# Performance work log

Hardware: AMD Instinct MI355X
Metric: run time of the kernel (lower is better)

## Reference

```python
import jax, jax.numpy as jnp
import numpy as np

GRID_SIZE = 5
SPLINE_ORDER = 3
NUM_BASIS = GRID_SIZE + SPLINE_ORDER  # 8
BN_EPS = 1e-5


def make_grid():
    # efficient_kan extended uniform grid on [-1, 1]
    h = 2.0 / GRID_SIZE
    return (jnp.arange(-SPLINE_ORDER, GRID_SIZE + SPLINE_ORDER + 1, dtype=jnp.float32) * h) - 1.0


def b_splines(x, grid):
    """Cox-de Boor B-spline bases. x: (...,) -> (..., NUM_BASIS)."""
    x = x[..., None]
    bases = ((x >= grid[:-1]) & (x < grid[1:])).astype(x.dtype)
    for p in range(1, SPLINE_ORDER + 1):
        left = (x - grid[: -(p + 1)]) / (grid[p:-1] - grid[: -(p + 1)])
        right = (grid[p + 1:] - x) / (grid[p + 1:] - grid[1:-p])
        bases = left * bases[..., :-1] + right * bases[..., 1:]
    return bases


def grouped_conv(x, w, groups, padding):
    return jax.lax.conv_general_dilated(
        x, w, window_strides=(1, 1), padding=[(padding, padding)] * 2,
        feature_group_count=groups,
        dimension_numbers=("NCHW", "OIHW", "NCHW"))


def kan_conv(x, w_base, b_base, w_spline, grid, groups, padding):
    # base branch: grouped conv on SiLU(x)
    base = grouped_conv(jax.nn.silu(x), w_base, groups, padding)
    base = base + b_base[None, :, None, None]
    # spline branch: per-channel B-spline basis expansion (C -> C*NUM_BASIS)
    B, C, H, W = x.shape
    sp = b_splines(jnp.moveaxis(x, 1, -1), grid)            # (B,H,W,C,NB)
    sp = jnp.moveaxis(sp.reshape(B, H, W, C * NUM_BASIS), -1, 1)  # (B,C*NB,H,W)
    return base + grouped_conv(sp, w_spline, groups, padding)


def setup_inputs() -> dict:
    key = jax.random.key(0)
    ks = jax.random.split(key, 8)
    B, C_in, C_out, G, H, W = 16, 128, 256, 8, 64, 64
    x = jax.random.normal(ks[0], (B, C_in, H, W), dtype=jnp.float32)
    w_base1 = jax.random.normal(ks[1], (C_out, C_in // G, 1, 1), jnp.float32) * 0.1
    b_base1 = jnp.zeros((C_out,), jnp.float32)
    w_spline1 = jax.random.normal(ks[2], (C_out, (C_in * NUM_BASIS) // G, 1, 1), jnp.float32) * 0.05
    w_base2 = jax.random.normal(ks[3], (C_out, C_out // G, 3, 3), jnp.float32) * 0.05
    b_base2 = jnp.zeros((C_out,), jnp.float32)
    w_spline2 = jax.random.normal(ks[4], (C_out, (C_out * NUM_BASIS) // G, 3, 3), jnp.float32) * 0.02
    gamma = jnp.ones((C_out,), jnp.float32)
    beta = jnp.zeros((C_out,), jnp.float32)
    return {"x": x, "w_base1": w_base1, "b_base1": b_base1, "w_spline1": w_spline1,
            "w_base2": w_base2, "b_base2": b_base2, "w_spline2": w_spline2,
            "gamma": gamma, "beta": beta}


def reference(x, w_base1, b_base1, w_spline1, w_base2, b_base2, w_spline2, gamma, beta):
    G = 8
    grid = make_grid()
    h = kan_conv(x, w_base1, b_base1, w_spline1, grid, G, padding=0)   # 1x1 grouped KAN conv
    h = kan_conv(h, w_base2, b_base2, w_spline2, grid, G, padding=1)   # 3x3 grouped KAN conv
    # BatchNorm2d (training mode: batch statistics over N,H,W)
    mean = jnp.mean(h, axis=(0, 2, 3), keepdims=True)
    var = jnp.var(h, axis=(0, 2, 3), keepdims=True)
    hn = (h - mean) * jax.lax.rsqrt(var + BN_EPS)
    return hn * gamma[None, :, None, None] + beta[None, :, None, None]
```

## Files before the change

### kernel.cpp

```cpp
#include <hip/hip_runtime.h>
#include <hip/hip_bf16.h>
#include <stdint.h>


#define NB 8
#define NF 9
#define CIN 128
#define COUT 256
#define GROUPS 8
#define HW 4096
#define BATCH 16

#define WFS_ELEMS 589824
#define WFB_ELEMS 73728
#define WF1S_ELEMS 32768
#define WF1B_ELEMS 8192

typedef __attribute__((ext_vector_type(8))) short bf16x8;
typedef __attribute__((ext_vector_type(4))) float f32x4;

__device__ __forceinline__ unsigned bf16r(float f) {
    union { float f; unsigned u; } c; c.f = f;
    unsigned r = c.u + 0x7FFF + ((c.u >> 16) & 1);
    return r >> 16;
}
__device__ __forceinline__ unsigned bfpack2(float lo, float hi) {
    unsigned r;
    asm("v_cvt_pk_bf16_f32 %0, %1, %2" : "=v"(r) : "v"(lo), "v"(hi));
    return r;
}
__device__ __forceinline__ unsigned bfpack2_typed(float lo, float hi) {
    __hip_bfloat16 a = __float2bfloat16(lo);
    __hip_bfloat16 b = __float2bfloat16(hi);
    unsigned short ua, ub;
    __builtin_memcpy(&ua, &a, 2);
    __builtin_memcpy(&ub, &b, 2);
    return (unsigned)ua | ((unsigned)ub << 16);
}

__device__ __forceinline__ float silu_fast(float v) {
    float e = __builtin_amdgcn_exp2f(v * -1.44269504088896f);
    return v * __builtin_amdgcn_rcpf(1.0f + e);
}

__device__ __forceinline__ void spline_w(float v, float& w0, float& w1,
                                         float& w2, float& w3, int& k) {
    float s = (v + 2.2f) * 2.5f;
    float fk = floorf(s);
    k = (int)fk;
    float u = s - fk;
    float um = 1.0f - u;
    float u2 = u * u, u3 = u2 * u;
    w0 = um * um * um * (1.0f / 6.0f);
    w1 = (3.0f * u3 - 6.0f * u2 + 4.0f) * (1.0f / 6.0f);
    w2 = (-3.0f * u3 + 3.0f * u2 + 3.0f * u + 1.0f) * (1.0f / 6.0f);
    w3 = u3 * (1.0f / 6.0f);
}

__device__ __forceinline__ uint4 spline_row(float v, bool in, float& sv) {
    sv = silu_fast(v);
    float w0, w1, w2, w3; int k;
    spline_w(v, w0, w1, w2, w3, k);
    unsigned W0 = bfpack2(w0, w1);
    unsigned W1 = bfpack2(w2, w3);
    int kk = in ? (k - 3) : 99;
    unsigned odd = (unsigned)kk & 1u;
    unsigned A = W0 << 16;
    unsigned B = (W0 >> 16) | (W1 << 16);
    unsigned C = W1 >> 16;
    unsigned t0 = odd ? A : W0;
    unsigned t1 = odd ? B : W1;
    unsigned t2 = odd ? C : 0u;
    int q = kk >> 1;
    uint4 pk;
    pk.x = (q == 0) ? t0 : (q == -1) ? t1 : (q == -2) ? t2 : 0u;
    pk.y = (q == 1) ? t0 : (q == 0)  ? t1 : (q == -1) ? t2 : 0u;
    pk.z = (q == 2) ? t0 : (q == 1)  ? t1 : (q == 0)  ? t2 : 0u;
    pk.w = (q == 3) ? t0 : (q == 2)  ? t1 : (q == 1)  ? t2 : 0u;
    return pk;
}

__device__ __forceinline__ void expand_u(int raw, bool in,
                                         uint4& pk, unsigned& su) {
    float v = __uint_as_float(((unsigned)raw) << 16);
    float sv;
    pk = spline_row(v, in, sv);
    su = bf16r(sv);
}

__global__ void __launch_bounds__(256) repack2_kernel(
    const float* __restrict__ wb1, const float* __restrict__ ws1,
    const float* __restrict__ wb2, const float* __restrict__ ws2,
    unsigned short* __restrict__ wfs, unsigned short* __restrict__ wfb,
    unsigned short* __restrict__ wf1s, unsigned short* __restrict__ wf1b) {
    int i = blockIdx.x * 256 + threadIdx.x;
    if (i < WF1S_ELEMS) {
        int j = i & 7;
        int lane = (i >> 3) & 63;
        int nf = (i >> 9) & 1;
        int cc = (i >> 10) & 3;
        int g = i >> 12;
        int c_loc = cc * 4 + (lane >> 4);
        int cog = g * 32 + nf * 16 + (lane & 15);
        wf1s[i] = (unsigned short)bf16r(ws1[cog * 128 + c_loc * 8 + j]);
    }
    if (i < WF1B_ELEMS) {
        int j = i & 7;
        int lane = (i >> 3) & 63;
        int nf = (i >> 9) & 1;
        int g = (i >> 10) & 7;
        int k = (lane >> 4) * 8 + j;
        int cog = g * 32 + nf * 16 + (lane & 15);
        wf1b[i] = (k < 16) ? (unsigned short)bf16r(wb1[cog * 16 + k]) : 0;
    }
    if (i < WFB_ELEMS) {
        int j = i & 7;
        int lane = (i >> 3) & 63;
        int nf = (i >> 9) & 1;
        int t = i >> 10;
        int dy = t % 3; t /= 3;
        int dx = t % 3; t /= 3;
        int g = t;
        int ch = (lane >> 4) * 8 + j;
        int cog = g * 32 + nf * 16 + (lane & 15);
        wfb[i] = (unsigned short)bf16r(wb2[((cog * 32 + ch) * 3 + dy) * 3 + dx]);
    }
    if (i < WFS_ELEMS) {
        int j = i & 7;
        int t = i >> 3;
        int lane = t & 63; t >>= 6;
        int nf = t & 1; t >>= 1;
        int dy = t % 3; t /= 3;
        int dx = t % 3; t /= 3;
        int cc = t & 7; t >>= 3;
        int g = t;
        int c_loc = cc * 4 + (lane >> 4);
        int cog = g * 32 + nf * 16 + (lane & 15);
        float v = ws2[((cog * 256 + c_loc * 8 + j) * 3 + dy) * 3 + dx];
        wfs[i] = (unsigned short)bf16r(v);
    }
}

__global__ void __launch_bounds__(256, 4) kan1m_kernel(
    const float* __restrict__ x, const bf16x8* __restrict__ wf1s,
    const bf16x8* __restrict__ wf1b, const float* __restrict__ bb1,
    unsigned short* __restrict__ h1) {
    __shared__ __align__(16) unsigned char lds[32768];
    unsigned char* spl = lds;
    unsigned char* slu = lds + 16384;

    const int tid = threadIdx.x;
    const int lane = tid & 63;
    const int w = tid >> 6;
    const int blk = blockIdx.x;
    const int tile = blk & 15;
    const int g = (blk >> 4) & 7;
    const int b = blk >> 7;
    const int lrow = lane & 15;
    const int lhi = lane >> 4;
    const int posg0 = tile * 256;

    {
        int key = (tid >> 1) & 3;
        uint4 z = {0, 0, 0, 0};
        *reinterpret_cast<uint4*>(slu + tid * 64 + ((2 ^ key) << 4)) = z;
        *reinterpret_cast<uint4*>(slu + tid * 64 + ((3 ^ key) << 4)) = z;
    }

    const float* xg = x + ((size_t)b * CIN + g * 16) * HW + posg0;

    float xreg[4];
#pragma unroll
    for (int it = 0; it < 4; ++it) xreg[it] = xg[it * HW + tid];

    f32x4 acc[4][2];
#pragma unroll
    for (int m = 0; m < 4; ++m)
#pragma unroll
        for (int nf = 0; nf < 2; ++nf) {
            float bias = bb1[g * 32 + nf * 16 + lrow];
            acc[m][nf] = (f32x4){bias, bias, bias, bias};
        }

    for (int cc = 0; cc < 4; ++cc) {
        __syncthreads();
        int key = (tid >> 1) & 3;
#pragma unroll
        for (int it = 0; it < 4; ++it) {
            float sv;
            uint4 pk = spline_row(xreg[it], true, sv);
            *reinterpret_cast<uint4*>(spl + tid * 64 + ((it ^ key) << 4)) = pk;
            int cg = cc * 4 + it;
            *reinterpret_cast<unsigned short*>(
                slu + tid * 64 + (((cg >> 3) ^ key) << 4) + (cg & 7) * 2) =
                (unsigned short)bf16r(sv);
        }
        if (cc < 3) {
#pragma unroll
            for (int it = 0; it < 4; ++it)
                xreg[it] = xg[((cc + 1) * 4 + it) * HW + tid];
        }
        __syncthreads();
        const bf16x8* wpc = wf1s + (size_t)((g * 4 + cc) * 2) * 64;
        bf16x8 bf0 = wpc[lane];
        bf16x8 bf1 = wpc[64 + lane];
#pragma unroll
        for (int m = 0; m < 4; ++m) {
            int pos = w * 64 + m * 16 + lrow;
            int ra = pos * 64 + ((lhi ^ ((pos >> 1) & 3)) << 4);
            bf16x8 af = *reinterpret_cast<const bf16x8*>(spl + ra);
            acc[m][0] = __builtin_amdgcn_mfma_f32_16x16x32_bf16(af, bf0, acc[m][0], 0, 0, 0);
            acc[m][1] = __builtin_amdgcn_mfma_f32_16x16x32_bf16(af, bf1, acc[m][1], 0, 0, 0);
        }
    }
    {
        const bf16x8* wpb = wf1b + (size_t)(g * 2) * 64;
        bf16x8 bf0 = wpb[lane];
        bf16x8 bf1 = wpb[64 + lane];
#pragma unroll
        for (int m = 0; m < 4; ++m) {
            int pos = w * 64 + m * 16 + lrow;
            int ra = pos * 64 + ((lhi ^ ((pos >> 1) & 3)) << 4);
            bf16x8 af = *reinterpret_cast<const bf16x8*>(slu + ra);
            acc[m][0] = __builtin_amdgcn_mfma_f32_16x16x32_bf16(af, bf0, acc[m][0], 0, 0, 0);
            acc[m][1] = __builtin_amdgcn_mfma_f32_16x16x32_bf16(af, bf1, acc[m][1], 0, 0, 0);
        }
    }
#pragma unroll
    for (int m = 0; m < 4; ++m)
#pragma unroll
        for (int nf = 0; nf < 2; ++nf) {
            int co = g * 32 + nf * 16 + lrow;
            size_t base = ((size_t)b * COUT + co) * HW + posg0 + w * 64 + m * 16 + lhi * 4;
            uint2 o = {bfpack2_typed(acc[m][nf][0], acc[m][nf][1]),
                       bfpack2_typed(acc[m][nf][2], acc[m][nf][3])};
            *reinterpret_cast<uint2*>(&h1[base]) = o;
        }
}

__device__ __forceinline__ void mfma_hr(
    const unsigned char* __restrict__ base, const int (&ra)[6],
    const bf16x8 (&bf)[3][2], f32x4 (&acc)[4][2]) {
#pragma unroll
    for (int hr = 0; hr < 6; ++hr) {
        bf16x8 af = *reinterpret_cast<const bf16x8*>(base + ra[hr]);
#pragma unroll
        for (int dy = 0; dy < 3; ++dy) {
            int y = hr - dy;
            if (y >= 0 && y < 4) {
                acc[y][0] = __builtin_amdgcn_mfma_f32_16x16x32_bf16(af, bf[dy][0], acc[y][0], 0, 0, 0);
                acc[y][1] = __builtin_amdgcn_mfma_f32_16x16x32_bf16(af, bf[dy][1], acc[y][1], 0, 0, 0);
            }
        }
    }
}

__global__ void __launch_bounds__(256, 3) kan2_mfma5_kernel(
    const unsigned short* __restrict__ h1, const bf16x8* __restrict__ wfs,
    const bf16x8* __restrict__ wfb, const float* __restrict__ bb2,
    unsigned short* __restrict__ hb, float* __restrict__ partial2) {
    __shared__ __align__(16) unsigned char lds[41472];
    unsigned char* spl = lds;
    unsigned char* slu = lds + 20736;

    const int tid = threadIdx.x;
    const int lane = tid & 63;
    const int w = tid >> 6;
    const int blk = blockIdx.x;
    const int tile = blk & 15;
    const int g = (blk >> 4) & 7;
    const int b = blk >> 7;
    const int ty = (tile >> 2) * 16, tx = (tile & 3) * 16;
    const int lrow = lane & 15;
    const int lhi = lane >> 4;

    int offv[6], wadS[6], sluB[6], keysh[6];
#pragma unroll
    for (int it = 0; it < 6; ++it) {
        int e = tid + it * 256;
        int ch = (e * 3237) >> 20;
        int p = e - ch * 324;
        int hy = (p * 57) >> 10;
        int hx = p - hy * 18;
        int iy = ty + hy - 1, ix = tx + hx - 1;
        bool in = ((unsigned)iy < 64u) & ((unsigned)ix < 64u);
        offv[it] = in ? (ch * HW + iy * 64 + ix) : -1;
        int key = (p >> 1) & 3;
        wadS[it] = p * 64 + ((ch ^ key) << 4);
        sluB[it] = p * 64 + ch * 2;
        keysh[it] = key << 4;
    }

    const int pbase0 = (w * 4) * 18 + lrow;
    int raA[3][6];
#pragma unroll
    for (int dx = 0; dx < 3; ++dx)
#pragma unroll
        for (int hr = 0; hr < 6; ++hr) {
            int p = pbase0 + dx + hr * 18;
            raA[dx][hr] = p * 64 + ((lhi ^ ((p >> 1) & 3)) << 4);
        }

    const unsigned short* h1g = h1 + (size_t)(b * COUT + g * 32) * HW;

    int vregU[6];
    uint4 ereg[6];
    unsigned sreg[6];
#pragma unroll
    for (int it = 0; it < 6; ++it)
        if (it < 5 || tid < 16)
            vregU[it] = (offv[it] >= 0) ? (int)h1g[offv[it]] : 0;
#pragma unroll
    for (int it = 0; it < 6; ++it)
        if (it < 5 || tid < 16)
            expand_u(vregU[it], offv[it] >= 0, ereg[it], sreg[it]);
#pragma unroll
    for (int it = 0; it < 6; ++it)
        if (it < 5 || tid < 16)
            vregU[it] = (offv[it] >= 0) ? (int)h1g[4 * HW + offv[it]] : 0;

    f32x4 acc[4][2];
#pragma unroll
    for (int y = 0; y < 4; ++y)
#pragma unroll
        for (int nf = 0; nf < 2; ++nf) {
            float bias = bb2[g * 32 + nf * 16 + lrow];
            acc[y][nf] = (f32x4){bias, bias, bias, bias};
        }

    const bf16x8* wl = wfs + (size_t)(g * 8) * 18 * 64 + lane;

    for (int cc = 0; cc < 8; ++cc) {
        bf16x8 bf0[3][2];
#pragma unroll
        for (int dy = 0; dy < 3; ++dy)
#pragma unroll
            for (int nf = 0; nf < 2; ++nf)
                bf0[dy][nf] = wl[(dy * 2 + nf) * 64];

        __syncthreads();
        {
            int t4 = (cc >> 1) << 4;
            int u8 = (cc & 1) << 3;
#pragma unroll
            for (int it = 0; it < 6; ++it)
                if (it < 5 || tid < 16) {
                    *reinterpret_cast<uint4*>(spl + wadS[it]) = ereg[it];
                    *reinterpret_cast<unsigned short*>(
                        slu + sluB[it] + (t4 ^ keysh[it]) + u8) =
                        (unsigned short)sreg[it];
                }
        }
        __syncthreads();

        bf16x8 bf1[3][2], bf2[3][2];
#pragma unroll
        for (int dy = 0; dy < 3; ++dy)
#pragma unroll
            for (int nf = 0; nf < 2; ++nf)
                bf1[dy][nf] = wl[(6 + dy * 2 + nf) * 64];
        __builtin_amdgcn_s_setprio(1);
        mfma_hr(spl, raA[0], bf0, acc);
        __builtin_amdgcn_s_setprio(0);
#pragma unroll
        for (int dy = 0; dy < 3; ++dy)
#pragma unroll
            for (int nf = 0; nf < 2; ++nf)
                bf2[dy][nf] = wl[(12 + dy * 2 + nf) * 64];
        __builtin_amdgcn_s_setprio(1);
        mfma_hr(spl, raA[1], bf1, acc);
        __builtin_amdgcn_s_setprio(0);
        if (cc < 7) {
#pragma unroll
            for (int it = 0; it < 6; ++it)
                if (it < 5 || tid < 16)
                    expand_u(vregU[it], offv[it] >= 0, ereg[it], sreg[it]);
        }
        if (cc < 6) {
#pragma unroll
            for (int it = 0; it < 6; ++it)
                if (it < 5 || tid < 16)
                    vregU[it] = (offv[it] >= 0)
                        ? (int)h1g[(size_t)((cc + 2) * 4) * HW + offv[it]] : 0;
        }
        __builtin_amdgcn_s_setprio(1);
        mfma_hr(spl, raA[2], bf2, acc);
        __builtin_amdgcn_s_setprio(0);
        wl += 18 * 64;
    }

    {
        const bf16x8* wlb = wfb + (size_t)(g * 3) * 6 * 64 + lane;
#pragma unroll
        for (int dx = 0; dx < 3; ++dx) {
            bf16x8 bf[3][2];
#pragma unroll
            for (int dy = 0; dy < 3; ++dy)
#pragma unroll
                for (int nf = 0; nf < 2; ++nf)
                    bf[dy][nf] = wlb[(dx * 6 + dy * 2 + nf) * 64];
            __builtin_amdgcn_s_setprio(1);
            mfma_hr(slu, raA[dx], bf, acc);
            __builtin_amdgcn_s_setprio(0);
        }
    }

#pragma unroll
    for (int y = 0; y < 4; ++y) {
        int oy = ty + w * 4 + y;
#pragma unroll
        for (int nf = 0; nf < 2; ++nf) {
            int co = g * 32 + nf * 16 + lrow;
            uint2 o = {bfpack2_typed(acc[y][nf][0], acc[y][nf][1]),
                       bfpack2_typed(acc[y][nf][2], acc[y][nf][3])};
            *reinterpret_cast<uint2*>(
                &hb[(((size_t)b * COUT + co) * 64 + oy) * 64 + tx + lhi * 4]) = o;
        }
    }

    float s0 = 0.0f, q0 = 0.0f, s1 = 0.0f, q1 = 0.0f;
#pragma unroll
    for (int y = 0; y < 4; ++y)
#pragma unroll
        for (int i = 0; i < 4; ++i) {
            float a0 = acc[y][0][i], a1 = acc[y][1][i];
            s0 += a0; q0 = fmaf(a0, a0, q0);
            s1 += a1; q1 = fmaf(a1, a1, q1);
        }
    s0 += __shfl_xor(s0, 16); s0 += __shfl_xor(s0, 32);
    q0 += __shfl_xor(q0, 16); q0 += __shfl_xor(q0, 32);
    s1 += __shfl_xor(s1, 16); s1 += __shfl_xor(s1, 32);
    q1 += __shfl_xor(q1, 16); q1 += __shfl_xor(q1, 32);
    __syncthreads();
    float* stb = reinterpret_cast<float*>(lds);
    if (lane < 16) {
        int base = (w * 16 + lane) * 4;
        stb[base] = s0; stb[base + 1] = q0;
        stb[base + 2] = s1; stb[base + 3] = q1;
    }
    __syncthreads();
    if (tid < 64) {
        int slot = tid >> 1;
        int j = tid & 1;
        int lr = slot & 15, nf = slot >> 4;
        float a = 0.0f;
#pragma unroll
        for (int wv = 0; wv < 4; ++wv)
            a += stb[(wv * 16 + lr) * 4 + nf * 2 + j];
        partial2[blk * 64 + tid] = a;
    }
}

__global__ void __launch_bounds__(256) bnstat2_kernel(
    const float* __restrict__ partial2, const float* __restrict__ gamma,
    const float* __restrict__ beta, float* __restrict__ stats) {
    int co = blockIdx.x;
    int t = threadIdx.x;
    int g = co >> 5, loc = co & 31;
    int b = t >> 4, tile = t & 15;
    int blk = (b * 8 + g) * 16 + tile;
    float s = partial2[blk * 64 + loc * 2];
    float ss = partial2[blk * 64 + loc * 2 + 1];
    __shared__ float r1[256], r2[256];
    r1[t] = s; r2[t] = ss;
    __syncthreads();
    for (int o = 128; o > 0; o >>= 1) {
        if (t < o) { r1[t] += r1[t + o]; r2[t] += r2[t + o]; }
        __syncthreads();
    }
    if (t == 0) {
        const float invn = 1.0f / 65536.0f;
        float mean = r1[0] * invn;
        float var = r2[0] * invn - mean * mean;
        float sc = gamma[co] * rsqrtf(var + 1e-5f);
        stats[2 * co] = sc;
        stats[2 * co + 1] = beta[co] - mean * sc;
    }
}

__global__ void __launch_bounds__(256) bnapply_kernel(
    const unsigned short* __restrict__ hb, const float* __restrict__ stats,
    float* __restrict__ out) {
    int i = blockIdx.x * 256 + threadIdx.x;
    int co = (i >> 9) & 255;
    float sc = stats[2 * co], sh = stats[2 * co + 1];
    uint4 v = *reinterpret_cast<const uint4*>(hb + (size_t)i * 8);
    float4 o0, o1;
    o0.x = fmaf(__uint_as_float(v.x << 16), sc, sh);
    o0.y = fmaf(__uint_as_float(v.x & 0xFFFF0000u), sc, sh);
    o0.z = fmaf(__uint_as_float(v.y << 16), sc, sh);
    o0.w = fmaf(__uint_as_float(v.y & 0xFFFF0000u), sc, sh);
    o1.x = fmaf(__uint_as_float(v.z << 16), sc, sh);
    o1.y = fmaf(__uint_as_float(v.z & 0xFFFF0000u), sc, sh);
    o1.z = fmaf(__uint_as_float(v.w << 16), sc, sh);
    o1.w = fmaf(__uint_as_float(v.w & 0xFFFF0000u), sc, sh);
    float4* op = reinterpret_cast<float4*>(out + (size_t)i * 8);
    op[0] = o0;
    op[1] = o1;
}

extern "C" void kernel_launch(void* const* d_in, const int* in_sizes, int n_in,
                              void* d_out, int out_size, void* d_ws, size_t ws_size,
                              hipStream_t stream) {
    const float* x   = (const float*)d_in[0];
    const float* wb1 = (const float*)d_in[1];
    const float* bb1 = (const float*)d_in[2];
    const float* ws1 = (const float*)d_in[3];
    const float* wb2 = (const float*)d_in[4];
    const float* bb2 = (const float*)d_in[5];
    const float* ws2 = (const float*)d_in[6];
    const float* gamma = (const float*)d_in[7];
    const float* beta  = (const float*)d_in[8];

    char* ws = (char*)d_ws;
    unsigned short* wfs  = (unsigned short*)ws;
    unsigned short* wfb  = (unsigned short*)(ws + 1179648);
    unsigned short* wf1s = (unsigned short*)(ws + 1327104);
    unsigned short* wf1b = (unsigned short*)(ws + 1392640);
    float* partial2 = (float*)(ws + 1409024);
    float* stats    = (float*)(ws + 1933312);
    unsigned short* h1 = (unsigned short*)(ws + 1935360);
    unsigned short* hb = (unsigned short*)(ws + 35489792);

    repack2_kernel<<<(WFS_ELEMS + 255) / 256, 256, 0, stream>>>(
        wb1, ws1, wb2, ws2, wfs, wfb, wf1s, wf1b);
    kan1m_kernel<<<BATCH * GROUPS * 16, 256, 0, stream>>>(
        x, (const bf16x8*)wf1s, (const bf16x8*)wf1b, bb1, h1);
    kan2_mfma5_kernel<<<BATCH * GROUPS * 16, 256, 0, stream>>>(
        h1, (const bf16x8*)wfs, (const bf16x8*)wfb, bb2, hb, partial2);
    bnstat2_kernel<<<COUT, 256, 0, stream>>>(partial2, gamma, beta, stats);
    bnapply_kernel<<<8192, 256, 0, stream>>>(hb, stats, (float*)d_out);
}
```

Measured before the change: 148.6 us.

## Halve SiLU LDS buffer by splitting base-branch conv into two K16 MFMA passes

The SiLU staging buffer in LDS shrinks from 32 to 16 channels per pixel. The base-branch 3x3 conv is split into two halves: channels 0-15 run mid-loop at cc==3, before the buffer is overwritten, and channels 16-31 run after the loop. Both halves use 16x16x16 bf16 MFMAs, and the base weights are repacked to match. The smaller LDS footprint allows launch bounds of 4 blocks per CU instead of 3. The cost is more, smaller MFMA instructions and tighter register limits.

```diff
diff --git a/kernel.cpp b/kernel.cpp
--- a/kernel.cpp
+++ b/kernel.cpp
@@ -17,6 +17,7 @@
 #define WF1B_ELEMS 8192
 
 typedef __attribute__((ext_vector_type(8))) short bf16x8;
+typedef __attribute__((ext_vector_type(4))) short bf16x4;
 typedef __attribute__((ext_vector_type(4))) float f32x4;
 
 __device__ __forceinline__ unsigned bf16r(float f) {
@@ -36,6 +37,15 @@
     __builtin_memcpy(&ua, &a, 2);
     __builtin_memcpy(&ub, &b, 2);
     return (unsigned)ua | ((unsigned)ub << 16);
+}
+
+__device__ __forceinline__ f32x4 mfma16(bf16x4 a, bf16x4 b, f32x4 c) {
+#if __has_builtin(__builtin_amdgcn_mfma_f32_16x16x16bf16_1k)
+    return __builtin_amdgcn_mfma_f32_16x16x16bf16_1k(a, b, c, 0, 0, 0);
+#else
+    asm("v_mfma_f32_16x16x16_bf16 %0, %1, %2, %0" : "+v"(c) : "v"(a), "v"(b));
+    return c;
+#endif
 }
 
 __device__ __forceinline__ float silu_fast(float v) {
@@ -114,14 +124,15 @@
         wf1b[i] = (k < 16) ? (unsigned short)bf16r(wb1[cog * 16 + k]) : 0;
     }
     if (i < WFB_ELEMS) {
-        int j = i & 7;
-        int lane = (i >> 3) & 63;
-        int nf = (i >> 9) & 1;
-        int t = i >> 10;
+        int j = i & 3;
+        int lane = (i >> 2) & 63;
+        int nf = (i >> 8) & 1;
+        int t = i >> 9;
         int dy = t % 3; t /= 3;
         int dx = t % 3; t /= 3;
+        int half = t & 1; t >>= 1;
         int g = t;
-        int ch = (lane >> 4) * 8 + j;
+        int ch = half * 16 + (lane >> 4) * 4 + j;
         int cog = g * 32 + nf * 16 + (lane & 15);
         wfb[i] = (unsigned short)bf16r(wb2[((cog * 32 + ch) * 3 + dy) * 3 + dx]);
     }
@@ -255,11 +266,11 @@
     }
 }
 
-__global__ void __launch_bounds__(256, 3) kan2_mfma5_kernel(
+__global__ void __launch_bounds__(256, 4) kan2_mfma6_kernel(
     const unsigned short* __restrict__ h1, const bf16x8* __restrict__ wfs,
-    const bf16x8* __restrict__ wfb, const float* __restrict__ bb2,
+    const bf16x4* __restrict__ wfb, const float* __restrict__ bb2,
     unsigned short* __restrict__ hb, float* __restrict__ partial2) {
-    __shared__ __align__(16) unsigned char lds[41472];
+    __shared__ __align__(16) unsigned char lds[31104];
     unsigned char* spl = lds;
     unsigned char* slu = lds + 20736;
 
@@ -274,7 +285,7 @@
     const int lrow = lane & 15;
     const int lhi = lane >> 4;
 
-    int offv[6], wadS[6], sluB[6], keysh[6];
+    int offv[6], wadS[6], sluB[6], keysh3[6];
 #pragma unroll
     for (int it = 0; it < 6; ++it) {
         int e = tid + it * 256;
@@ -287,18 +298,20 @@
         offv[it] = in ? (ch * HW + iy * 64 + ix) : -1;
         int key = (p >> 1) & 3;
         wadS[it] = p * 64 + ((ch ^ key) << 4);
-        sluB[it] = p * 64 + ch * 2;
-        keysh[it] = key << 4;
+        sluB[it] = p * 32 + ch * 2;
+        keysh3[it] = key << 3;
     }
 
     const int pbase0 = (w * 4) * 18 + lrow;
-    int raA[3][6];
+    int raA[3][6], raB[3][6];
 #pragma unroll
     for (int dx = 0; dx < 3; ++dx)
 #pragma unroll
         for (int hr = 0; hr < 6; ++hr) {
             int p = pbase0 + dx + hr * 18;
-            raA[dx][hr] = p * 64 + ((lhi ^ ((p >> 1) & 3)) << 4);
+            int key = (p >> 1) & 3;
+            raA[dx][hr] = p * 64 + ((lhi ^ key) << 4);
+            raB[dx][hr] = p * 32 + ((lhi ^ key) << 3);
         }
 
     const unsigned short* h1g = h1 + (size_t)(b * COUT + g * 32) * HW;
@@ -340,14 +353,13 @@
 
         __syncthreads();
         {
-            int t4 = (cc >> 1) << 4;
-            int u8 = (cc & 1) << 3;
+            int t8 = (cc & 3) << 3;
 #pragma unroll
             for (int it = 0; it < 6; ++it)
                 if (it < 5 || tid < 16) {
                     *reinterpret_cast<uint4*>(spl + wadS[it]) = ereg[it];
                     *reinterpret_cast<unsigned short*>(
-                        slu + sluB[it] + (t4 ^ keysh[it]) + u8) =
+                        slu + sluB[it] + (t8 ^ keysh3[it])) =
                         (unsigned short)sreg[it];
                 }
         }
@@ -386,21 +398,56 @@
         __builtin_amdgcn_s_setprio(1);
         mfma_hr(spl, raA[2], bf2, acc);
         __builtin_amdgcn_s_setprio(0);
+        if (cc == 3) {
+#pragma unroll
+            for (int dx = 0; dx < 3; ++dx) {
+                bf16x4 bf[3][2];
+#pragma unroll
+                for (int dy = 0; dy < 3; ++dy)
+#pragma unroll
+                    for (int nf = 0; nf < 2; ++nf)
+                        bf[dy][nf] = wfb[((((g * 2 + 0) * 3 + dx) * 3 + dy) * 2 + nf) * 64 + lane];
+                __builtin_amdgcn_s_setprio(1);
+#pragma unroll
+                for (int hr = 0; hr < 6; ++hr) {
+                    bf16x4 af = *reinterpret_cast<const bf16x4*>(slu + raB[dx][hr]);
+#pragma unroll
+                    for (int dy = 0; dy < 3; ++dy) {
+                        int y = hr - dy;
+                        if (y >= 0 && y < 4) {
+                            acc[y][0] = mfma16(af, bf[dy][0], acc[y][0]);
+                            acc[y][1] = mfma16(af, bf[dy][1], acc[y][1]);
+                        }
+                    }
+                }
+                __builtin_amdgcn_s_setprio(0);
+            }
+        }
         wl += 18 * 64;
     }
 
     {
-        const bf16x8* wlb = wfb + (size_t)(g * 3) * 6 * 64 + lane;
 #pragma unroll
         for (int dx = 0; dx < 3; ++dx) {
-            bf16x8 bf[3][2];
+            bf16x4 bf[3][2];
 #pragma unroll
             for (int dy = 0; dy < 3; ++dy)
 #pragma unroll
                 for (int nf = 0; nf < 2; ++nf)
-                    bf[dy][nf] = wlb[(dx * 6 + dy * 2 + nf) * 64];
+                    bf[dy][nf] = wfb[((((g * 2 + 1) * 3 + dx) * 3 + dy) * 2 + nf) * 64 + lane];
             __builtin_amdgcn_s_setprio(1);
-            mfma_hr(slu, raA[dx], bf, acc);
+#pragma unroll
+            for (int hr = 0; hr < 6; ++hr) {
+                bf16x4 af = *reinterpret_cast<const bf16x4*>(slu + raB[dx][hr]);
+#pragma unroll
+                for (int dy = 0; dy < 3; ++dy) {
+                    int y = hr - dy;
+                    if (y >= 0 && y < 4) {
+                        acc[y][0] = mfma16(af, bf[dy][0], acc[y][0]);
+                        acc[y][1] = mfma16(af, bf[dy][1], acc[y][1]);
+                    }
+                }
+            }
             __builtin_amdgcn_s_setprio(0);
         }
     }
@@ -526,8 +573,8 @@
         wb1, ws1, wb2, ws2, wfs, wfb, wf1s, wf1b);
     kan1m_kernel<<<BATCH * GROUPS * 16, 256, 0, stream>>>(
         x, (const bf16x8*)wf1s, (const bf16x8*)wf1b, bb1, h1);
-    kan2_mfma5_kernel<<<BATCH * GROUPS * 16, 256, 0, stream>>>(
-        h1, (const bf16x8*)wfs, (const bf16x8*)wfb, bb2, hb, partial2);
+    kan2_mfma6_kernel<<<BATCH * GROUPS * 16, 256, 0, stream>>>(
+        h1, (const bf16x8*)wfs, (const bf16x4*)wfb, bb2, hb, partial2);
     bnstat2_kernel<<<COUT, 256, 0, stream>>>(partial2, gamma, beta, stats);
     bnapply_kernel<<<8192, 256, 0, stream>>>(hb, stats, (float*)d_out);
 }
```

Result: slower. 513.1 us (+245.2%).
